# Kernel tuning notes

Hardware: AMD Instinct MI355X
Metric: run time of the kernel (lower is better)

The kernel has to match this reference:

```python
import jax, jax.numpy as jnp
import numpy as np

DEPTH = 11  # tree depth -> depth+1 routing steps, n_nodes = 2**(DEPTH+1)-1 = 4095


def setup_inputs() -> dict:
    key = jax.random.key(0)
    k1, k2, k3 = jax.random.split(key, 3)
    B, D_in, D_out = 8192, 2048, 2048
    n_nodes = 2 ** (DEPTH + 1) - 1
    x = jax.random.normal(k1, (B, D_in), dtype=jnp.float32)
    # nn.Linear(input_width, n_nodes, bias=False).weight : (n_nodes, D_in)
    W_in = jax.random.normal(k2, (n_nodes, D_in), dtype=jnp.float32) / np.sqrt(D_in).astype(np.float32)
    # nn.Linear(n_nodes, output_width, bias=False).weight : (D_out, n_nodes)
    W_out = jax.random.normal(k3, (D_out, n_nodes), dtype=jnp.float32) / np.sqrt(n_nodes).astype(np.float32)
    return {"x": x, "W_in": W_in, "W_out": W_out}


def reference(x, W_in, W_out):
    B = x.shape[0]
    # Torch loop recomputes linear_in(x) every step; the result is identical each
    # iteration, so compute the (B, n_nodes) logits once and gather per depth step.
    logits_all = x @ W_in.T  # (B, n_nodes)

    def step(cur, _):
        # gather the logit of each sample's current tree node
        score = jnp.take_along_axis(logits_all, cur[:, None], axis=1)[:, 0]  # (B,)
        nxt = cur * 2 + (score >= 0).astype(jnp.int32) + 1  # left/right child
        return nxt, (cur, score)

    init = jnp.zeros((B,), dtype=jnp.int32)
    _, (nodes, scores) = jax.lax.scan(step, init, None, length=DEPTH + 1)
    nodes = nodes.T    # (B, depth+1) visited node ids
    scores = scores.T  # (B, depth+1) selected logits

    mlp1 = jax.nn.gelu(scores, approximate=False)  # exact GELU, matches nn.GELU
    # Conditional output projection: only the depth+1 visited columns of W_out
    # contribute per sample (FFF / conditional-MoE semantics).
    W_sel = W_out.T[nodes]  # (B, depth+1, D_out)
    return jnp.einsum('bd,bdo->bo', mlp1, W_sel)
```

## Files before the change

kernel.cpp:

```cpp
#include <hip/hip_runtime.h>
#include <math.h>

#define B_SZ   8192
#define D_IN   2048
#define D_OUT  2048
#define N_NODES 4095
#define STEPS  12

__global__ __launch_bounds__(256) void transpose_wout(
    const float* __restrict__ W, float* __restrict__ Wt) {
  __shared__ float tile[32][33];
  const int tx = threadIdx.x;
  const int ty = threadIdx.y;
  const int col0 = blockIdx.x * 32;
  const int row0 = blockIdx.y * 32;

  #pragma unroll
  for (int i = ty; i < 32; i += 8) {
    const int c = col0 + tx;
    float v = 0.0f;
    if (c < N_NODES) v = W[(size_t)(row0 + i) * N_NODES + c];
    tile[i][tx] = v;
  }
  __syncthreads();
  #pragma unroll
  for (int i = ty; i < 32; i += 8) {
    const int r = col0 + i;
    if (r < N_NODES) Wt[(size_t)r * D_OUT + row0 + tx] = tile[tx][i];
  }
}

__global__ __launch_bounds__(256) void route_kernel(
    const float* __restrict__ x, const float* __restrict__ W_in,
    int* __restrict__ nodes, float* __restrict__ gsc) {
  const int wave = (int)((blockIdx.x * (size_t)blockDim.x + threadIdx.x) >> 6);
  const int lane = threadIdx.x & 63;
  if (wave >= B_SZ) return;

  const float* xr = x + (size_t)wave * D_IN;
  float xv[D_IN / 64];
  #pragma unroll
  for (int i = 0; i < D_IN / 64; ++i) xv[i] = xr[lane + i * 64];

  int cur = 0;
  #pragma unroll
  for (int d = 0; d < STEPS; ++d) {
    const float* wr = W_in + (size_t)cur * D_IN;
    float s = 0.0f;
    #pragma unroll
    for (int i = 0; i < D_IN / 64; ++i) s += xv[i] * wr[lane + i * 64];
    #pragma unroll
    for (int off = 32; off > 0; off >>= 1) s += __shfl_xor(s, off);

    if (lane == 0) {
      nodes[wave * STEPS + d] = cur;
      gsc[wave * STEPS + d] = 0.5f * s * (1.0f + erff(s * 0.70710678118654752f));
    }
    cur = cur * 2 + ((s >= 0.0f) ? 2 : 1);
  }
}

__global__ __launch_bounds__(256) void out_kernel(
    const float* __restrict__ Wt, const int* __restrict__ nodes,
    const float* __restrict__ gsc, float* __restrict__ out) {
  const int b = blockIdx.x;
  const int t = threadIdx.x;

  __shared__ int   s_nodes[STEPS];
  __shared__ float s_g[STEPS];
  if (t < STEPS) {
    s_nodes[t] = nodes[b * STEPS + t];
    s_g[t]     = gsc[b * STEPS + t];
  }
  __syncthreads();

  float4 acc0 = make_float4(0.f, 0.f, 0.f, 0.f);
  float4 acc1 = make_float4(0.f, 0.f, 0.f, 0.f);

  #pragma unroll
  for (int d = 0; d < STEPS; ++d) {
    const float4* wr = (const float4*)(Wt + (size_t)s_nodes[d] * D_OUT);
    const float g = s_g[d];
    const float4 w0 = wr[t];
    const float4 w1 = wr[256 + t];
    acc0.x += g * w0.x; acc0.y += g * w0.y; acc0.z += g * w0.z; acc0.w += g * w0.w;
    acc1.x += g * w1.x; acc1.y += g * w1.y; acc1.z += g * w1.z; acc1.w += g * w1.w;
  }

  float4* op = (float4*)(out + (size_t)b * D_OUT);
  op[t]       = acc0;
  op[256 + t] = acc1;
}

extern "C" void kernel_launch(void* const* d_in, const int* in_sizes, int n_in,
                              void* d_out, int out_size, void* d_ws, size_t ws_size,
                              hipStream_t stream) {
  const float* x     = (const float*)d_in[0];
  const float* W_in  = (const float*)d_in[1];
  const float* W_out = (const float*)d_in[2];
  float* out = (float*)d_out;

  float* Wt   = (float*)d_ws;
  int*   nodes = (int*)((char*)d_ws + (size_t)N_NODES * D_OUT * sizeof(float));
  float* gsc   = (float*)((char*)nodes + (size_t)B_SZ * STEPS * sizeof(int));

  {
    dim3 blk(32, 8);
    dim3 grd((N_NODES + 31) / 32, D_OUT / 32);
    transpose_wout<<<grd, blk, 0, stream>>>(W_out, Wt);
  }
  {
    dim3 blk(256);
    dim3 grd(B_SZ / 4);
    route_kernel<<<grd, blk, 0, stream>>>(x, W_in, nodes, gsc);
  }
  {
    dim3 blk(256);
    dim3 grd(B_SZ);
    out_kernel<<<grd, blk, 0, stream>>>(Wt, nodes, gsc, out);
  }
}
```

Before: 253.1 us.

## Group samples by leaf so each block reuses the shared path's W_out rows

The output stage now launches one block per leaf instead of one per sample. Each block scans all leaf assignments to collect the samples that reached its leaf, loads the 12 path columns of transposed W_out into registers once, and computes every matching sample's output from them. The router also switches to float4 loads and stores only the leaf index rather than the full node list. This cuts redundant W_out gathers, but each block rescans all 8192 leaf entries, uses a 32 KB shared list, and load balance depends on how samples spread across leaves.

```diff
diff --git a/kernel.cpp b/kernel.cpp
--- a/kernel.cpp
+++ b/kernel.cpp
@@ -1,11 +1,12 @@
 #include <hip/hip_runtime.h>
 #include <math.h>
 
-#define B_SZ   8192
-#define D_IN   2048
-#define D_OUT  2048
+#define B_SZ    8192
+#define D_IN    2048
+#define D_OUT   2048
 #define N_NODES 4095
-#define STEPS  12
+#define STEPS   12
+#define N_LEAVES 2048
 
 __global__ __launch_bounds__(256) void transpose_wout(
     const float* __restrict__ W, float* __restrict__ Wt) {
@@ -32,64 +33,81 @@
 
 __global__ __launch_bounds__(256) void route_kernel(
     const float* __restrict__ x, const float* __restrict__ W_in,
-    int* __restrict__ nodes, float* __restrict__ gsc) {
+    int* __restrict__ leafArr, float* __restrict__ gsc) {
   const int wave = (int)((blockIdx.x * (size_t)blockDim.x + threadIdx.x) >> 6);
   const int lane = threadIdx.x & 63;
   if (wave >= B_SZ) return;
 
-  const float* xr = x + (size_t)wave * D_IN;
-  float xv[D_IN / 64];
+  const float4* xr = (const float4*)(x + (size_t)wave * D_IN);
+  float4 xv[8];
   #pragma unroll
-  for (int i = 0; i < D_IN / 64; ++i) xv[i] = xr[lane + i * 64];
+  for (int i = 0; i < 8; ++i) xv[i] = xr[lane + i * 64];
 
   int cur = 0;
   #pragma unroll
   for (int d = 0; d < STEPS; ++d) {
-    const float* wr = W_in + (size_t)cur * D_IN;
+    const float4* wr = (const float4*)(W_in + (size_t)cur * D_IN);
     float s = 0.0f;
     #pragma unroll
-    for (int i = 0; i < D_IN / 64; ++i) s += xv[i] * wr[lane + i * 64];
+    for (int i = 0; i < 8; ++i) {
+      const float4 w = wr[lane + i * 64];
+      s += xv[i].x * w.x + xv[i].y * w.y + xv[i].z * w.z + xv[i].w * w.w;
+    }
     #pragma unroll
     for (int off = 32; off > 0; off >>= 1) s += __shfl_xor(s, off);
 
     if (lane == 0) {
-      nodes[wave * STEPS + d] = cur;
       gsc[wave * STEPS + d] = 0.5f * s * (1.0f + erff(s * 0.70710678118654752f));
+      if (d == STEPS - 1) leafArr[wave] = cur - 2047;
     }
     cur = cur * 2 + ((s >= 0.0f) ? 2 : 1);
   }
 }
 
 __global__ __launch_bounds__(256) void out_kernel(
-    const float* __restrict__ Wt, const int* __restrict__ nodes,
+    const float* __restrict__ Wt, const int* __restrict__ leafArr,
     const float* __restrict__ gsc, float* __restrict__ out) {
-  const int b = blockIdx.x;
+  __shared__ int list[B_SZ];
+  __shared__ int cnt;
+  const int l = blockIdx.x;
   const int t = threadIdx.x;
 
-  __shared__ int   s_nodes[STEPS];
-  __shared__ float s_g[STEPS];
-  if (t < STEPS) {
-    s_nodes[t] = nodes[b * STEPS + t];
-    s_g[t]     = gsc[b * STEPS + t];
+  if (t == 0) cnt = 0;
+  __syncthreads();
+  for (int b = t; b < B_SZ; b += 256)
+    if (leafArr[b] == l) list[atomicAdd(&cnt, 1)] = b;
+  __syncthreads();
+  const int n = cnt;
+  if (n == 0) return;
+
+  int path[STEPS];
+  {
+    int nd = l + 2047;
+    #pragma unroll
+    for (int d = STEPS - 1; d >= 0; --d) { path[d] = nd; nd = (nd - 1) >> 1; }
   }
-  __syncthreads();
-
-  float4 acc0 = make_float4(0.f, 0.f, 0.f, 0.f);
-  float4 acc1 = make_float4(0.f, 0.f, 0.f, 0.f);
 
   #pragma unroll
-  for (int d = 0; d < STEPS; ++d) {
-    const float4* wr = (const float4*)(Wt + (size_t)s_nodes[d] * D_OUT);
-    const float g = s_g[d];
-    const float4 w0 = wr[t];
-    const float4 w1 = wr[256 + t];
-    acc0.x += g * w0.x; acc0.y += g * w0.y; acc0.z += g * w0.z; acc0.w += g * w0.w;
-    acc1.x += g * w1.x; acc1.y += g * w1.y; acc1.z += g * w1.z; acc1.w += g * w1.w;
+  for (int c = 0; c < 2; ++c) {
+    const int col = c * 1024 + t * 4;
+    float4 w[STEPS];
+    #pragma unroll
+    for (int d = 0; d < STEPS; ++d)
+      w[d] = *(const float4*)(Wt + (size_t)path[d] * D_OUT + col);
+
+    for (int s = 0; s < n; ++s) {
+      const int b = list[s];
+      const float* g = gsc + (size_t)b * STEPS;
+      float4 acc = make_float4(0.f, 0.f, 0.f, 0.f);
+      #pragma unroll
+      for (int d = 0; d < STEPS; ++d) {
+        const float gd = g[d];
+        acc.x += gd * w[d].x; acc.y += gd * w[d].y;
+        acc.z += gd * w[d].z; acc.w += gd * w[d].w;
+      }
+      *(float4*)(out + (size_t)b * D_OUT + col) = acc;
+    }
   }
-
-  float4* op = (float4*)(out + (size_t)b * D_OUT);
-  op[t]       = acc0;
-  op[256 + t] = acc1;
 }
 
 extern "C" void kernel_launch(void* const* d_in, const int* in_sizes, int n_in,
@@ -100,9 +118,9 @@
   const float* W_out = (const float*)d_in[2];
   float* out = (float*)d_out;
 
-  float* Wt   = (float*)d_ws;
-  int*   nodes = (int*)((char*)d_ws + (size_t)N_NODES * D_OUT * sizeof(float));
-  float* gsc   = (float*)((char*)nodes + (size_t)B_SZ * STEPS * sizeof(int));
+  float* Wt      = (float*)d_ws;
+  int*   leafArr = (int*)((char*)d_ws + (size_t)N_NODES * D_OUT * sizeof(float));
+  float* gsc     = (float*)((char*)leafArr + (size_t)B_SZ * sizeof(int));
 
   {
     dim3 blk(32, 8);
@@ -112,11 +130,11 @@
   {
     dim3 blk(256);
     dim3 grd(B_SZ / 4);
-    route_kernel<<<grd, blk, 0, stream>>>(x, W_in, nodes, gsc);
+    route_kernel<<<grd, blk, 0, stream>>>(x, W_in, leafArr, gsc);
   }
   {
     dim3 blk(256);
-    dim3 grd(B_SZ);
-    out_kernel<<<grd, blk, 0, stream>>>(Wt, nodes, gsc, out);
+    dim3 grd(N_LEAVES);
+    out_kernel<<<grd, blk, 0, stream>>>(Wt, leafArr, gsc, out);
   }
 }
```

New measurement: 247.7 us. 2.1% less time.
